# Optimization experiments

Measured on AMD Instinct MI355X. Metric: run time of the kernel, lower is better.

The kernel has to match this reference:

```python
import math
import jax, jax.numpy as jnp
import numpy as np

B, CH3, T = 64, 192, 2048  # B = batch*heads, CH3 = 3*head_dim

def setup_inputs() -> dict:
    key = jax.random.key(0)
    qkv = jax.random.normal(key, (B, CH3, T), dtype=jnp.float32)
    return {"qkv": qkv}

def reference(qkv):
    ch = qkv.shape[1] // 3
    q, k, v = jnp.split(qkv, 3, axis=1)  # each [B, ch, T]
    scale = 1.0 / math.sqrt(math.sqrt(ch))
    # scores [B, T(query), S(key)]
    weight = jnp.einsum('bct,bcs->bts', q * scale, k * scale)
    weight = jax.nn.softmax(weight.astype(jnp.float32), axis=-1).astype(weight.dtype)
    return jnp.einsum('bts,bcs->bct', weight, v)
```

## Files before the change

### kernel.cpp

```cpp
#include <hip/hip_runtime.h>
#include <hip/hip_bf16.h>


#define DHEAD 64
#define TLEN  2048
#define NB    64
#define BQ    256
#define BK    64
#define LDA   72

typedef short s16x8 __attribute__((ext_vector_type(8)));
typedef float f32x4 __attribute__((ext_vector_type(4)));
typedef unsigned short u16x4 __attribute__((ext_vector_type(4)));
typedef unsigned short u16x8 __attribute__((ext_vector_type(8)));

__device__ __forceinline__ unsigned short f2bf(float f) {
    unsigned int u = __float_as_uint(f);
    u += 0x7fffu + ((u >> 16) & 1u);
    return (unsigned short)(u >> 16);
}

__global__ __launch_bounds__(256)
void prep(const float* __restrict__ qkv, unsigned short* __restrict__ ws) {
    const int tile   = blockIdx.x;
    const int tensor = blockIdx.y;
    const int b      = blockIdx.z;
    const int tid    = threadIdx.x;
    const float* src = qkv + ((size_t)b * 3 * DHEAD + tensor * DHEAD) * TLEN + tile * 64;
    unsigned short* qt = ws;
    unsigned short* kt = ws + (size_t)NB * DHEAD * TLEN;
    unsigned short* vd = kt + (size_t)NB * DHEAD * TLEN;

    if (tensor == 2) {
        unsigned short* dst = vd + (size_t)b * DHEAD * TLEN + tile * 64;
        int c = tid >> 4, t4 = (tid & 15) * 4;
        #pragma unroll
        for (int rr = 0; rr < 4; ++rr, c += 16) {
            float4 f = *(const float4*)(src + c * TLEN + t4);
            u16x4 p = {f2bf(f.x), f2bf(f.y), f2bf(f.z), f2bf(f.w)};
            *(u16x4*)(dst + (size_t)c * TLEN + t4) = p;
        }
    } else {
        __shared__ unsigned short T[64 * LDA];
        int c = tid >> 4, t4 = (tid & 15) * 4;
        #pragma unroll
        for (int rr = 0; rr < 4; ++rr, c += 16) {
            float4 f = *(const float4*)(src + c * TLEN + t4);
            T[(t4 + 0) * LDA + c] = f2bf(f.x);
            T[(t4 + 1) * LDA + c] = f2bf(f.y);
            T[(t4 + 2) * LDA + c] = f2bf(f.z);
            T[(t4 + 3) * LDA + c] = f2bf(f.w);
        }
        __syncthreads();
        unsigned short* dst = (tensor == 0 ? qt : kt) + (size_t)b * DHEAD * TLEN
                              + (size_t)tile * 64 * DHEAD;
        #pragma unroll
        for (int rep = 0; rep < 2; ++rep) {
            int idx = rep * 256 + tid;
            int t = idx >> 3, j = idx & 7;
            *(u16x8*)(dst + t * DHEAD + j * 8) = *(const u16x8*)(&T[t * LDA + j * 8]);
        }
    }
}

__global__ __launch_bounds__(256, 2)
void attn(const unsigned short* __restrict__ ws, float* __restrict__ out) {
    __shared__ unsigned short Ks[64 * LDA];
    __shared__ unsigned short Vs[64 * LDA];
    __shared__ unsigned short Pt[4][64 * LDA];

    const int tid  = threadIdx.x;
    const int wave = tid >> 6;
    const int lane = tid & 63;
    const int quad = lane >> 4;
    const int c16  = lane & 15;

    const int b  = blockIdx.y;
    const int t0 = blockIdx.x * BQ;

    const unsigned short* qt = ws + (size_t)b * DHEAD * TLEN + (size_t)(t0 + wave * 64) * DHEAD;
    const unsigned short* kt = ws + (size_t)NB * DHEAD * TLEN + (size_t)b * DHEAD * TLEN;
    const unsigned short* vd = ws + (size_t)2 * NB * DHEAD * TLEN + (size_t)b * DHEAD * TLEN;

    s16x8 qf[4][2];
    #pragma unroll
    for (int ts = 0; ts < 4; ++ts)
        #pragma unroll
        for (int kk = 0; kk < 2; ++kk)
            qf[ts][kk] = *(const s16x8*)(qt + (size_t)(ts * 16 + c16) * DHEAD + kk * 32 + quad * 8);

    f32x4 acco[4][4];
    #pragma unroll
    for (int i = 0; i < 4; ++i)
        #pragma unroll
        for (int j = 0; j < 4; ++j) acco[i][j] = f32x4{0.f, 0.f, 0.f, 0.f};
    float lp[4] = {0.f, 0.f, 0.f, 0.f};

    unsigned short* Pw = Pt[wave];

    u16x8 kc[2], vc[2];
    {
        #pragma unroll
        for (int r = 0; r < 2; ++r) {
            int id = tid + r * 256;
            kc[r] = *(const u16x8*)(kt + (size_t)id * 8);
            int c = id >> 3, j = id & 7;
            vc[r] = *(const u16x8*)(vd + (size_t)c * TLEN + j * 8);
        }
    }

    for (int it = 0; it < TLEN / BK; ++it) {
        __syncthreads();
        #pragma unroll
        for (int r = 0; r < 2; ++r) {
            int id = tid + r * 256;
            *(u16x8*)(&Ks[(id >> 3) * LDA + (id & 7) * 8]) = kc[r];
            *(u16x8*)(&Vs[(id >> 3) * LDA + (id & 7) * 8]) = vc[r];
        }
        __syncthreads();

        if (it + 1 < TLEN / BK) {
            int s0 = (it + 1) * BK;
            #pragma unroll
            for (int r = 0; r < 2; ++r) {
                int id = tid + r * 256;
                kc[r] = *(const u16x8*)(kt + (size_t)s0 * DHEAD + id * 8);
                int c = id >> 3, j = id & 7;
                vc[r] = *(const u16x8*)(vd + (size_t)c * TLEN + s0 + j * 8);
            }
        }

        f32x4 accs[4][4];
        #pragma unroll
        for (int i = 0; i < 4; ++i)
            #pragma unroll
            for (int j = 0; j < 4; ++j) accs[i][j] = f32x4{0.f, 0.f, 0.f, 0.f};
        #pragma unroll
        for (int kk = 0; kk < 2; ++kk)
            #pragma unroll
            for (int st = 0; st < 4; ++st) {
                s16x8 ka = *(const s16x8*)(&Ks[(st * 16 + c16) * LDA + kk * 32 + quad * 8]);
                #pragma unroll
                for (int ts = 0; ts < 4; ++ts)
                    accs[st][ts] = __builtin_amdgcn_mfma_f32_16x16x32_bf16(ka, qf[ts][kk], accs[st][ts], 0, 0, 0);
            }

        #pragma unroll
        for (int st = 0; st < 4; ++st)
            #pragma unroll
            for (int ts = 0; ts < 4; ++ts) {
                f32x4 v = accs[st][ts];
                float e0 = __expf(v[0] * 0.125f);
                float e1 = __expf(v[1] * 0.125f);
                float e2 = __expf(v[2] * 0.125f);
                float e3 = __expf(v[3] * 0.125f);
                lp[ts] += (e0 + e1) + (e2 + e3);
                u16x4 p = {f2bf(e0), f2bf(e1), f2bf(e2), f2bf(e3)};
                *(u16x4*)(&Pw[(ts * 16 + c16) * LDA + st * 16 + quad * 4]) = p;
            }

        #pragma unroll
        for (int kk = 0; kk < 2; ++kk) {
            s16x8 pb[4];
            #pragma unroll
            for (int ts = 0; ts < 4; ++ts)
                pb[ts] = *(const s16x8*)(&Pw[(ts * 16 + c16) * LDA + kk * 32 + quad * 8]);
            #pragma unroll
            for (int cst = 0; cst < 4; ++cst) {
                s16x8 va = *(const s16x8*)(&Vs[(cst * 16 + c16) * LDA + kk * 32 + quad * 8]);
                #pragma unroll
                for (int ts = 0; ts < 4; ++ts)
                    acco[cst][ts] = __builtin_amdgcn_mfma_f32_16x16x32_bf16(va, pb[ts], acco[cst][ts], 0, 0, 0);
            }
        }
    }

    float rinv[4];
    #pragma unroll
    for (int ts = 0; ts < 4; ++ts) {
        float l = lp[ts];
        l += __shfl_xor(l, 16);
        l += __shfl_xor(l, 32);
        rinv[ts] = 1.0f / l;
    }

    float* ob = out + (size_t)b * DHEAD * TLEN + t0 + wave * 64;
    #pragma unroll
    for (int cst = 0; cst < 4; ++cst)
        #pragma unroll
        for (int ts = 0; ts < 4; ++ts)
            #pragma unroll
            for (int r = 0; r < 4; ++r)
                ob[(size_t)(cst * 16 + quad * 4 + r) * TLEN + ts * 16 + c16] = acco[cst][ts][r] * rinv[ts];
}

extern "C" void kernel_launch(void* const* d_in, const int* in_sizes, int n_in,
                              void* d_out, int out_size, void* d_ws, size_t ws_size,
                              hipStream_t stream) {
    const float* qkv = (const float*)d_in[0];
    unsigned short* ws = (unsigned short*)d_ws;
    float* out = (float*)d_out;
    prep<<<dim3(TLEN / 64, 3, NB), 256, 0, stream>>>(qkv, ws);
    attn<<<dim3(TLEN / BQ, NB), 256, 0, stream>>>(ws, out);
}
```

Measured before the change: 252.1 us.

## Double-buffer K/V tiles in LDS and split prep into separate Q/K and V kernels

The attention loop now uses two LDS buffers for K/V and keeps two register prefetch sets, so each step needs a single barrier and global loads are issued two tiles ahead. The prep stage is split into a transpose kernel for Q/K that stages fp32 in LDS with odd padding, and a wider straight-copy kernel for V. Conversion now uses packed bf16 pairs. The aim is to hide global load latency and cut barrier overhead. The cost is more LDS and more registers under the 2-blocks-per-CU launch bound, plus one extra kernel launch.

```diff
diff --git a/kernel.cpp b/kernel.cpp
--- a/kernel.cpp
+++ b/kernel.cpp
@@ -8,6 +8,7 @@
 #define BQ    256
 #define BK    64
 #define LDA   72
+#define LDT   65
 
 typedef short s16x8 __attribute__((ext_vector_type(8)));
 typedef float f32x4 __attribute__((ext_vector_type(4)));
@@ -20,54 +21,141 @@
     return (unsigned short)(u >> 16);
 }
 
+__device__ __forceinline__ unsigned int cvt_pk_bf16(float a, float b) {
+    return (unsigned int)f2bf(a) | ((unsigned int)f2bf(b) << 16);
+}
+
 __global__ __launch_bounds__(256)
-void prep(const float* __restrict__ qkv, unsigned short* __restrict__ ws) {
-    const int tile   = blockIdx.x;
-    const int tensor = blockIdx.y;
-    const int b      = blockIdx.z;
-    const int tid    = threadIdx.x;
-    const float* src = qkv + ((size_t)b * 3 * DHEAD + tensor * DHEAD) * TLEN + tile * 64;
-    unsigned short* qt = ws;
-    unsigned short* kt = ws + (size_t)NB * DHEAD * TLEN;
-    unsigned short* vd = kt + (size_t)NB * DHEAD * TLEN;
-
-    if (tensor == 2) {
-        unsigned short* dst = vd + (size_t)b * DHEAD * TLEN + tile * 64;
+void prep_qk(const float* __restrict__ qkv, unsigned short* __restrict__ ws) {
+    __shared__ float T32[64 * LDT];
+    const int tile = blockIdx.x, tensor = blockIdx.y, b = blockIdx.z;
+    const int tid = threadIdx.x;
+    const float* src = qkv + ((size_t)b * 3 + tensor) * DHEAD * TLEN + tile * 64;
+    unsigned short* dst = ws + (size_t)tensor * NB * DHEAD * TLEN
+                        + (size_t)b * DHEAD * TLEN + (size_t)tile * 64 * DHEAD;
+    {
         int c = tid >> 4, t4 = (tid & 15) * 4;
         #pragma unroll
         for (int rr = 0; rr < 4; ++rr, c += 16) {
             float4 f = *(const float4*)(src + c * TLEN + t4);
-            u16x4 p = {f2bf(f.x), f2bf(f.y), f2bf(f.z), f2bf(f.w)};
-            *(u16x4*)(dst + (size_t)c * TLEN + t4) = p;
-        }
-    } else {
-        __shared__ unsigned short T[64 * LDA];
-        int c = tid >> 4, t4 = (tid & 15) * 4;
-        #pragma unroll
-        for (int rr = 0; rr < 4; ++rr, c += 16) {
-            float4 f = *(const float4*)(src + c * TLEN + t4);
-            T[(t4 + 0) * LDA + c] = f2bf(f.x);
-            T[(t4 + 1) * LDA + c] = f2bf(f.y);
-            T[(t4 + 2) * LDA + c] = f2bf(f.z);
-            T[(t4 + 3) * LDA + c] = f2bf(f.w);
-        }
-        __syncthreads();
-        unsigned short* dst = (tensor == 0 ? qt : kt) + (size_t)b * DHEAD * TLEN
-                              + (size_t)tile * 64 * DHEAD;
-        #pragma unroll
-        for (int rep = 0; rep < 2; ++rep) {
-            int idx = rep * 256 + tid;
-            int t = idx >> 3, j = idx & 7;
-            *(u16x8*)(dst + t * DHEAD + j * 8) = *(const u16x8*)(&T[t * LDA + j * 8]);
+            T32[(t4 + 0) * LDT + c] = f.x;
+            T32[(t4 + 1) * LDT + c] = f.y;
+            T32[(t4 + 2) * LDT + c] = f.z;
+            T32[(t4 + 3) * LDT + c] = f.w;
+        }
+    }
+    __syncthreads();
+    #pragma unroll
+    for (int rep = 0; rep < 2; ++rep) {
+        int idx = rep * 256 + tid;
+        int t = idx >> 3, j = idx & 7;
+        const float* row = &T32[t * LDT + j * 8];
+        union { u16x8 v; unsigned int u[4]; } o;
+        o.u[0] = cvt_pk_bf16(row[0], row[1]);
+        o.u[1] = cvt_pk_bf16(row[2], row[3]);
+        o.u[2] = cvt_pk_bf16(row[4], row[5]);
+        o.u[3] = cvt_pk_bf16(row[6], row[7]);
+        *(u16x8*)(dst + t * DHEAD + j * 8) = o.v;
+    }
+}
+
+__global__ __launch_bounds__(256)
+void prep_v(const float* __restrict__ qkv, unsigned short* __restrict__ ws) {
+    const int tile = blockIdx.x, b = blockIdx.y;
+    const int tid = threadIdx.x;
+    const float* src = qkv + ((size_t)b * 3 + 2) * DHEAD * TLEN + tile * 256;
+    unsigned short* dst = ws + (size_t)2 * NB * DHEAD * TLEN
+                        + (size_t)b * DHEAD * TLEN + tile * 256;
+    int c = tid >> 5, t8 = (tid & 31) * 8;
+    #pragma unroll
+    for (int rr = 0; rr < 8; ++rr, c += 8) {
+        float4 f0 = *(const float4*)(src + c * TLEN + t8);
+        float4 f1 = *(const float4*)(src + c * TLEN + t8 + 4);
+        union { u16x8 v; unsigned int u[4]; } o;
+        o.u[0] = cvt_pk_bf16(f0.x, f0.y);
+        o.u[1] = cvt_pk_bf16(f0.z, f0.w);
+        o.u[2] = cvt_pk_bf16(f1.x, f1.y);
+        o.u[3] = cvt_pk_bf16(f1.z, f1.w);
+        *(u16x8*)(dst + c * TLEN + t8) = o.v;
+    }
+}
+
+__device__ __forceinline__ void loadkv(const unsigned short* kt, const unsigned short* vd,
+                                       int s0, u16x8 kc[2], u16x8 vc[2], int tid) {
+    #pragma unroll
+    for (int r = 0; r < 2; ++r) {
+        int id = tid + r * 256;
+        kc[r] = *(const u16x8*)(kt + (size_t)s0 * DHEAD + id * 8);
+        vc[r] = *(const u16x8*)(vd + (size_t)(id >> 3) * TLEN + s0 + (id & 7) * 8);
+    }
+}
+
+__device__ __forceinline__ void stage(unsigned short* K, unsigned short* V,
+                                      const u16x8 kc[2], const u16x8 vc[2], int tid) {
+    #pragma unroll
+    for (int r = 0; r < 2; ++r) {
+        int id = tid + r * 256;
+        *(u16x8*)(&K[(id >> 3) * LDA + (id & 7) * 8]) = kc[r];
+        *(u16x8*)(&V[(id >> 3) * LDA + (id & 7) * 8]) = vc[r];
+    }
+}
+
+__device__ __forceinline__ void compute_tile(const unsigned short* Ks, const unsigned short* Vs,
+                                             unsigned short* Pw,
+                                             const s16x8 (&qf)[4][2], f32x4 (&acco)[4][4],
+                                             float (&lp)[4], int quad, int c16) {
+    f32x4 accs[4][4];
+    #pragma unroll
+    for (int i = 0; i < 4; ++i)
+        #pragma unroll
+        for (int j = 0; j < 4; ++j) accs[i][j] = f32x4{0.f, 0.f, 0.f, 0.f};
+    #pragma unroll
+    for (int kk = 0; kk < 2; ++kk)
+        #pragma unroll
+        for (int st = 0; st < 4; ++st) {
+            s16x8 ka = *(const s16x8*)(&Ks[(st * 16 + c16) * LDA + kk * 32 + quad * 8]);
+            #pragma unroll
+            for (int ts = 0; ts < 4; ++ts)
+                accs[st][ts] = __builtin_amdgcn_mfma_f32_16x16x32_bf16(ka, qf[ts][kk], accs[st][ts], 0, 0, 0);
+        }
+
+    #pragma unroll
+    for (int st = 0; st < 4; ++st)
+        #pragma unroll
+        for (int ts = 0; ts < 4; ++ts) {
+            f32x4 v = accs[st][ts];
+            float e0 = __expf(v[0] * 0.125f);
+            float e1 = __expf(v[1] * 0.125f);
+            float e2 = __expf(v[2] * 0.125f);
+            float e3 = __expf(v[3] * 0.125f);
+            lp[ts] += (e0 + e1) + (e2 + e3);
+            union { u16x4 v4; unsigned int u[2]; } p;
+            p.u[0] = cvt_pk_bf16(e0, e1);
+            p.u[1] = cvt_pk_bf16(e2, e3);
+            *(u16x4*)(&Pw[(ts * 16 + c16) * LDA + st * 16 + quad * 4]) = p.v4;
+        }
+
+    #pragma unroll
+    for (int kk = 0; kk < 2; ++kk) {
+        s16x8 pb[4];
+        #pragma unroll
+        for (int ts = 0; ts < 4; ++ts)
+            pb[ts] = *(const s16x8*)(&Pw[(ts * 16 + c16) * LDA + kk * 32 + quad * 8]);
+        #pragma unroll
+        for (int cst = 0; cst < 4; ++cst) {
+            s16x8 va = *(const s16x8*)(&Vs[(cst * 16 + c16) * LDA + kk * 32 + quad * 8]);
+            #pragma unroll
+            for (int ts = 0; ts < 4; ++ts)
+                acco[cst][ts] = __builtin_amdgcn_mfma_f32_16x16x32_bf16(va, pb[ts], acco[cst][ts], 0, 0, 0);
         }
     }
 }
 
 __global__ __launch_bounds__(256, 2)
 void attn(const unsigned short* __restrict__ ws, float* __restrict__ out) {
-    __shared__ unsigned short Ks[64 * LDA];
-    __shared__ unsigned short Vs[64 * LDA];
-    __shared__ unsigned short Pt[4][64 * LDA];
+    __shared__ alignas(16) unsigned short Ks2[2][64 * LDA];
+    __shared__ alignas(16) unsigned short Vs2[2][64 * LDA];
+    __shared__ alignas(16) unsigned short Pt[4][64 * LDA];
 
     const int tid  = threadIdx.x;
     const int wave = tid >> 6;
@@ -98,81 +186,20 @@
 
     unsigned short* Pw = Pt[wave];
 
-    u16x8 kc[2], vc[2];
-    {
-        #pragma unroll
-        for (int r = 0; r < 2; ++r) {
-            int id = tid + r * 256;
-            kc[r] = *(const u16x8*)(kt + (size_t)id * 8);
-            int c = id >> 3, j = id & 7;
-            vc[r] = *(const u16x8*)(vd + (size_t)c * TLEN + j * 8);
-        }
-    }
-
-    for (int it = 0; it < TLEN / BK; ++it) {
+    u16x8 kcA[2], vcA[2], kcB[2], vcB[2];
+    loadkv(kt, vd, 0, kcA, vcA, tid);
+    loadkv(kt, vd, BK, kcB, vcB, tid);
+
+    for (int it = 0; it < TLEN / BK; it += 2) {
+        stage(Ks2[0], Vs2[0], kcA, vcA, tid);
         __syncthreads();
-        #pragma unroll
-        for (int r = 0; r < 2; ++r) {
-            int id = tid + r * 256;
-            *(u16x8*)(&Ks[(id >> 3) * LDA + (id & 7) * 8]) = kc[r];
-            *(u16x8*)(&Vs[(id >> 3) * LDA + (id & 7) * 8]) = vc[r];
-        }
+        if (it + 2 < TLEN / BK) loadkv(kt, vd, (it + 2) * BK, kcA, vcA, tid);
+        compute_tile(Ks2[0], Vs2[0], Pw, qf, acco, lp, quad, c16);
+
+        stage(Ks2[1], Vs2[1], kcB, vcB, tid);
         __syncthreads();
-
-        if (it + 1 < TLEN / BK) {
-            int s0 = (it + 1) * BK;
-            #pragma unroll
-            for (int r = 0; r < 2; ++r) {
-                int id = tid + r * 256;
-                kc[r] = *(const u16x8*)(kt + (size_t)s0 * DHEAD + id * 8);
-                int c = id >> 3, j = id & 7;
-                vc[r] = *(const u16x8*)(vd + (size_t)c * TLEN + s0 + j * 8);
-            }
-        }
-
-        f32x4 accs[4][4];
-        #pragma unroll
-        for (int i = 0; i < 4; ++i)
-            #pragma unroll
-            for (int j = 0; j < 4; ++j) accs[i][j] = f32x4{0.f, 0.f, 0.f, 0.f};
-        #pragma unroll
-        for (int kk = 0; kk < 2; ++kk)
-            #pragma unroll
-            for (int st = 0; st < 4; ++st) {
-                s16x8 ka = *(const s16x8*)(&Ks[(st * 16 + c16) * LDA + kk * 32 + quad * 8]);
-                #pragma unroll
-                for (int ts = 0; ts < 4; ++ts)
-                    accs[st][ts] = __builtin_amdgcn_mfma_f32_16x16x32_bf16(ka, qf[ts][kk], accs[st][ts], 0, 0, 0);
-            }
-
-        #pragma unroll
-        for (int st = 0; st < 4; ++st)
-            #pragma unroll
-            for (int ts = 0; ts < 4; ++ts) {
-                f32x4 v = accs[st][ts];
-                float e0 = __expf(v[0] * 0.125f);
-                float e1 = __expf(v[1] * 0.125f);
-                float e2 = __expf(v[2] * 0.125f);
-                float e3 = __expf(v[3] * 0.125f);
-                lp[ts] += (e0 + e1) + (e2 + e3);
-                u16x4 p = {f2bf(e0), f2bf(e1), f2bf(e2), f2bf(e3)};
-                *(u16x4*)(&Pw[(ts * 16 + c16) * LDA + st * 16 + quad * 4]) = p;
-            }
-
-        #pragma unroll
-        for (int kk = 0; kk < 2; ++kk) {
-            s16x8 pb[4];
-            #pragma unroll
-            for (int ts = 0; ts < 4; ++ts)
-                pb[ts] = *(const s16x8*)(&Pw[(ts * 16 + c16) * LDA + kk * 32 + quad * 8]);
-            #pragma unroll
-            for (int cst = 0; cst < 4; ++cst) {
-                s16x8 va = *(const s16x8*)(&Vs[(cst * 16 + c16) * LDA + kk * 32 + quad * 8]);
-                #pragma unroll
-                for (int ts = 0; ts < 4; ++ts)
-                    acco[cst][ts] = __builtin_amdgcn_mfma_f32_16x16x32_bf16(va, pb[ts], acco[cst][ts], 0, 0, 0);
-            }
-        }
+        if (it + 3 < TLEN / BK) loadkv(kt, vd, (it + 3) * BK, kcB, vcB, tid);
+        compute_tile(Ks2[1], Vs2[1], Pw, qf, acco, lp, quad, c16);
     }
 
     float rinv[4];
@@ -200,6 +227,7 @@
     const float* qkv = (const float*)d_in[0];
     unsigned short* ws = (unsigned short*)d_ws;
     float* out = (float*)d_out;
-    prep<<<dim3(TLEN / 64, 3, NB), 256, 0, stream>>>(qkv, ws);
+    prep_qk<<<dim3(TLEN / 64, 2, NB), 256, 0, stream>>>(qkv, ws);
+    prep_v<<<dim3(TLEN / 256, NB), 256, 0, stream>>>(qkv, ws);
     attn<<<dim3(TLEN / BQ, NB), 256, 0, stream>>>(ws, out);
 }
```

Result: slower. 271.6 us (+7.7%).
